# Kernel optimization log

Hardware: AMD Instinct MI355X
Metric: run time of the kernel (lower is better)

Reference implementation:

```python
import jax, jax.numpy as jnp
import numpy as np
import math

B, T, C, H, DFF = 4, 2048, 1024, 16, 4096
HD = C // H
EPS = 1e-5


def _layernorm(x, g, b):
    mu = jnp.mean(x, axis=-1, keepdims=True)
    var = jnp.var(x, axis=-1, keepdims=True)
    return (x - mu) * jax.lax.rsqrt(var + EPS) * g + b


def _new_gelu(x):
    # 0.5*x*(1+tanh(sqrt(2/pi)*(x+0.044715*x^3)))
    c = math.sqrt(2.0 / math.pi)
    return 0.5 * x * (1.0 + jnp.tanh(c * (x + 0.044715 * x ** 3)))


def setup_inputs() -> dict:
    key = jax.random.key(0)
    ks = jax.random.split(key, 12)
    s = lambda fan_in: 1.0 / math.sqrt(fan_in)
    return {
        "x": jax.random.normal(ks[0], (B, T, C), jnp.float32),
        "ln1_g": jnp.ones((C,), jnp.float32),
        "ln1_b": jnp.zeros((C,), jnp.float32),
        "w_qkv": jax.random.normal(ks[1], (C, 3 * C), jnp.float32) * s(C),
        "b_qkv": jnp.zeros((3 * C,), jnp.float32),
        "w_o": jax.random.normal(ks[2], (C, C), jnp.float32) * s(C),
        "b_o": jnp.zeros((C,), jnp.float32),
        "ln2_g": jnp.ones((C,), jnp.float32),
        "ln2_b": jnp.zeros((C,), jnp.float32),
        "w_fc": jax.random.normal(ks[3], (C, DFF), jnp.float32) * s(C),
        "b_fc": jnp.zeros((DFF,), jnp.float32),
        "w_proj": jax.random.normal(ks[4], (DFF, C), jnp.float32) * s(DFF),
        "b_proj": jnp.zeros((C,), jnp.float32),
    }


def reference(x, ln1_g, ln1_b, w_qkv, b_qkv, w_o, b_o, ln2_g, ln2_b, w_fc, b_fc, w_proj, b_proj):
    # --- attention sub-block ---
    h = _layernorm(x, ln1_g, ln1_b)
    qkv = h @ w_qkv + b_qkv                                  # (B,T,3C)
    q, k, v = jnp.split(qkv, 3, axis=-1)
    q = q.reshape(B, T, H, HD).transpose(0, 2, 1, 3)          # (B,H,T,hd)
    k = k.reshape(B, T, H, HD).transpose(0, 2, 1, 3)
    v = v.reshape(B, T, H, HD).transpose(0, 2, 1, 3)
    scores = jnp.einsum("bhqd,bhkd->bhqk", q, k) / math.sqrt(HD)
    causal = jnp.tril(jnp.ones((T, T), jnp.bool_))            # (T,T)
    scores = jnp.where(causal[None, None], scores, -jnp.inf)
    probs = jax.nn.softmax(scores, axis=-1)
    attn = jnp.einsum("bhqk,bhkd->bhqd", probs, v)
    attn = attn.transpose(0, 2, 1, 3).reshape(B, T, C)
    x = x + attn @ w_o + b_o
    # --- MLP sub-block ---
    h2 = _layernorm(x, ln2_g, ln2_b)
    x = x + _new_gelu(h2 @ w_fc + b_fc) @ w_proj + b_proj
    return x
```

## Files before the change

kernel.cpp:

```cpp
#include <hip/hip_runtime.h>
#include <hip/hip_bf16.h>

using bf16 = __hip_bfloat16;
typedef __attribute__((ext_vector_type(8))) short bf16x8;
typedef __attribute__((ext_vector_type(4))) float f32x4;
typedef __attribute__((ext_vector_type(16))) float f32x16;

#define LOG2E 1.4426950408889634f

__device__ inline short f2b(float f) {
  __hip_bfloat16 h = __float2bfloat16(f);
  return *reinterpret_cast<short*>(&h);
}
__device__ inline float b2f(short s) {
  unsigned int u = ((unsigned int)(unsigned short)s) << 16;
  float f;
  __builtin_memcpy(&f, &u, 4);
  return f;
}
__device__ inline unsigned pk2(float a, float b) {
  return (unsigned)(unsigned short)f2b(a) |
         ((unsigned)(unsigned short)f2b(b) << 16);
}

__global__ __launch_bounds__(256) void transpose_cast_kernel(
    const float* __restrict__ in, bf16* __restrict__ out, int K, int N) {
  __shared__ float tile[32][33];
  int tx = threadIdx.x & 31;
  int ty = threadIdx.x >> 5;
  int n0 = blockIdx.x * 32, k0 = blockIdx.y * 32;
#pragma unroll
  for (int i = 0; i < 4; i++)
    tile[ty + i * 8][tx] = in[(size_t)(k0 + ty + i * 8) * N + n0 + tx];
  __syncthreads();
#pragma unroll
  for (int i = 0; i < 4; i++)
    out[(size_t)(n0 + ty + i * 8) * K + k0 + tx] =
        __float2bfloat16(tile[tx][ty + i * 8]);
}

__global__ __launch_bounds__(256) void transpose_v_kernel(
    const bf16* __restrict__ qkv, bf16* __restrict__ vt) {
  __shared__ short tile[64][66];
  const int bh = blockIdx.y;
  const int b = bh >> 4, h = bh & 15;
  const int t0 = blockIdx.x * 64;
  const int tid = threadIdx.x;
  const int r = tid >> 3, c8 = (tid & 7) * 8;
#pragma unroll
  for (int p = 0; p < 2; p++) {
    int t = r + p * 32;
    bf16x8 v = *(const bf16x8*)&qkv[(size_t)(b * 2048 + t0 + t) * 3072 + 2048 +
                                    h * 64 + c8];
#pragma unroll
    for (int i = 0; i < 8; i++) tile[t][c8 + i] = v[i];
  }
  __syncthreads();
#pragma unroll
  for (int p = 0; p < 2; p++) {
    int d = r + p * 32;
    int tt = c8;
    bf16x8 o;
#pragma unroll
    for (int i = 0; i < 8; i++) o[i] = tile[tt + i][d];
    *(bf16x8*)&vt[(size_t)(bh * 64 + d) * 2048 + t0 + tt] = o;
  }
}

__global__ __launch_bounds__(256) void ln_kernel(
    const float* __restrict__ x, const float* __restrict__ g,
    const float* __restrict__ b, bf16* __restrict__ out) {
  int row = blockIdx.x;
  const float4 v = ((const float4*)(x + (size_t)row * 1024))[threadIdx.x];
  float s = v.x + v.y + v.z + v.w;
  float ss = v.x * v.x + v.y * v.y + v.z * v.z + v.w * v.w;
#pragma unroll
  for (int off = 1; off < 64; off <<= 1) {
    s += __shfl_xor(s, off);
    ss += __shfl_xor(ss, off);
  }
  __shared__ float red[2][4];
  int w = threadIdx.x >> 6, lane = threadIdx.x & 63;
  if (lane == 0) { red[0][w] = s; red[1][w] = ss; }
  __syncthreads();
  s = red[0][0] + red[0][1] + red[0][2] + red[0][3];
  ss = red[1][0] + red[1][1] + red[1][2] + red[1][3];
  float mu = s * (1.0f / 1024.0f);
  float var = ss * (1.0f / 1024.0f) - mu * mu;
  float rstd = rsqrtf(var + 1e-5f);
  const float4 gv = ((const float4*)g)[threadIdx.x];
  const float4 bv = ((const float4*)b)[threadIdx.x];
  short4 o4;
  o4.x = f2b((v.x - mu) * rstd * gv.x + bv.x);
  o4.y = f2b((v.y - mu) * rstd * gv.y + bv.y);
  o4.z = f2b((v.z - mu) * rstd * gv.z + bv.z);
  o4.w = f2b((v.w - mu) * rstd * gv.w + bv.w);
  ((short4*)out)[(size_t)row * 256 + threadIdx.x] = o4;
}

__global__ __launch_bounds__(256) void fused_ln_kernel(
    const float* __restrict__ p0, const float* __restrict__ p1,
    const float* __restrict__ bo, const float* __restrict__ x,
    const float* __restrict__ g, const float* __restrict__ bln,
    float* __restrict__ x1, bf16* __restrict__ h2) {
  int row = blockIdx.x;
  size_t base = (size_t)row * 256 + threadIdx.x;
  float4 a = ((const float4*)p0)[base];
  float4 c = ((const float4*)p1)[base];
  float4 xr = ((const float4*)x)[base];
  float4 bo4 = ((const float4*)bo)[threadIdx.x];
  float4 v;
  v.x = a.x + c.x + xr.x + bo4.x;
  v.y = a.y + c.y + xr.y + bo4.y;
  v.z = a.z + c.z + xr.z + bo4.z;
  v.w = a.w + c.w + xr.w + bo4.w;
  ((float4*)x1)[base] = v;
  float s = v.x + v.y + v.z + v.w;
  float ss = v.x * v.x + v.y * v.y + v.z * v.z + v.w * v.w;
#pragma unroll
  for (int off = 1; off < 64; off <<= 1) {
    s += __shfl_xor(s, off);
    ss += __shfl_xor(ss, off);
  }
  __shared__ float red[2][4];
  int w = threadIdx.x >> 6, lane = threadIdx.x & 63;
  if (lane == 0) { red[0][w] = s; red[1][w] = ss; }
  __syncthreads();
  s = red[0][0] + red[0][1] + red[0][2] + red[0][3];
  ss = red[1][0] + red[1][1] + red[1][2] + red[1][3];
  float mu = s * (1.0f / 1024.0f);
  float var = ss * (1.0f / 1024.0f) - mu * mu;
  float rstd = rsqrtf(var + 1e-5f);
  const float4 gv = ((const float4*)g)[threadIdx.x];
  const float4 bv = ((const float4*)bln)[threadIdx.x];
  short4 o4;
  o4.x = f2b((v.x - mu) * rstd * gv.x + bv.x);
  o4.y = f2b((v.y - mu) * rstd * gv.y + bv.y);
  o4.z = f2b((v.z - mu) * rstd * gv.z + bv.z);
  o4.w = f2b((v.w - mu) * rstd * gv.w + bv.w);
  ((short4*)h2)[base] = o4;
}

__global__ __launch_bounds__(256) void fused_add_kernel(
    float* __restrict__ out, const float* __restrict__ q1,
    const float* __restrict__ x1, const float* __restrict__ bp, int n4) {
  for (int i = blockIdx.x * 256 + threadIdx.x; i < n4; i += gridDim.x * 256) {
    float4 a = ((const float4*)out)[i];
    float4 c = ((const float4*)q1)[i];
    float4 xr = ((const float4*)x1)[i];
    float4 b4 = ((const float4*)bp)[i & 255];
    float4 v;
    v.x = a.x + c.x + xr.x + b4.x;
    v.y = a.y + c.y + xr.y + b4.y;
    v.z = a.z + c.z + xr.z + b4.z;
    v.w = a.w + c.w + xr.w + b4.w;
    ((float4*)out)[i] = v;
  }
}

template <int EPI>
__global__ __launch_bounds__(512, 1) void gemm256_kernel(
    const bf16* __restrict__ A, const bf16* __restrict__ Bt,
    const float* __restrict__ bias, float* __restrict__ out0,
    float* __restrict__ out1, void* __restrict__ outv, int M, int N, int Kfull,
    int Ksub, int ntiles) {
  __shared__ short As[2][256 * 64];
  __shared__ short Bs[2][256 * 64];
  const int tid = threadIdx.x;
  const int lane = tid & 63, wid = tid >> 6;
  const int wr = wid >> 2, wc = wid & 3;

  const int nwg = gridDim.x;
  const int flat = blockIdx.x;
  const int sw = (flat & 7) * (nwg >> 3) + (flat >> 3);
  const int kq = sw / ntiles;
  const int tile = sw % ntiles;
  const int gy = M >> 8;
  const int bcol = tile / gy, brow = tile % gy;
  const int koff = kq * Ksub;
  const int nk = Ksub >> 6;

  const int srow = tid >> 3;
  const int schs = (tid & 7) ^ (srow & 7);

  auto stA = [&](int kt, int buf) {
#pragma unroll
    for (int r = 0; r < 4; r++) {
      const bf16* src = A + (size_t)(brow * 256 + r * 64 + srow) * Kfull +
                        koff + kt * 64 + schs * 8;
      __builtin_amdgcn_global_load_lds(
          (const __attribute__((address_space(1))) unsigned int*)src,
          (__attribute__((address_space(3))) unsigned int*)
              &As[buf][(r * 64 + wid * 8) * 64],
          16, 0, 0);
    }
  };
  auto stB = [&](int kt, int buf) {
#pragma unroll
    for (int r = 0; r < 4; r++) {
      const bf16* src = Bt + (size_t)(bcol * 256 + r * 64 + srow) * Kfull +
                        koff + kt * 64 + schs * 8;
      __builtin_amdgcn_global_load_lds(
          (const __attribute__((address_space(1))) unsigned int*)src,
          (__attribute__((address_space(3))) unsigned int*)
              &Bs[buf][(r * 64 + wid * 8) * 64],
          16, 0, 0);
    }
  };

  f32x4 acc[8][4] = {};
  bf16x8 af[4][2], bfr[4][2];

  auto rdB = [&](int cur) {
#pragma unroll
    for (int nn = 0; nn < 4; nn++)
#pragma unroll
      for (int ks = 0; ks < 2; ks++) {
        const int row = wc * 64 + nn * 16 + (lane & 15);
        const int ch = (ks * 4 + (lane >> 4)) ^ (row & 7);
        bfr[nn][ks] = *(const bf16x8*)&Bs[cur][row * 64 + ch * 8];
      }
  };
  auto rdA = [&](int cur, int mh) {
#pragma unroll
    for (int mm = 0; mm < 4; mm++)
#pragma unroll
      for (int ks = 0; ks < 2; ks++) {
        const int row = wr * 128 + mh * 64 + mm * 16 + (lane & 15);
        const int ch = (ks * 4 + (lane >> 4)) ^ (row & 7);
        af[mm][ks] = *(const bf16x8*)&As[cur][row * 64 + ch * 8];
      }
  };

  stA(0, 0);
  stB(0, 0);
  asm volatile("s_waitcnt vmcnt(0)" ::: "memory");
  __builtin_amdgcn_s_barrier();

  for (int t = 0; t < nk; t++) {
    const int cur = t & 1, nxt = cur ^ 1;
    rdB(cur);
    rdA(cur, 0);
    if (t + 1 < nk) {
      stA(t + 1, nxt);
      stB(t + 1, nxt);
    }
    __builtin_amdgcn_s_barrier();
    asm volatile("s_waitcnt lgkmcnt(0)" ::: "memory");
    __builtin_amdgcn_sched_barrier(0);
    __builtin_amdgcn_s_setprio(1);
#pragma unroll
    for (int mm = 0; mm < 4; mm++)
#pragma unroll
      for (int nn = 0; nn < 4; nn++)
#pragma unroll
        for (int ks = 0; ks < 2; ks++)
          acc[mm][nn] = __builtin_amdgcn_mfma_f32_16x16x32_bf16(
              af[mm][ks], bfr[nn][ks], acc[mm][nn], 0, 0, 0);
    __builtin_amdgcn_s_setprio(0);
    __builtin_amdgcn_s_barrier();
    rdA(cur, 1);
    asm volatile("s_waitcnt lgkmcnt(0)" ::: "memory");
    __builtin_amdgcn_sched_barrier(0);
    __builtin_amdgcn_s_setprio(1);
#pragma unroll
    for (int mm = 0; mm < 4; mm++)
#pragma unroll
      for (int nn = 0; nn < 4; nn++)
#pragma unroll
        for (int ks = 0; ks < 2; ks++)
          acc[4 + mm][nn] = __builtin_amdgcn_mfma_f32_16x16x32_bf16(
              af[mm][ks], bfr[nn][ks], acc[4 + mm][nn], 0, 0, 0);
    __builtin_amdgcn_s_setprio(0);
    if (t + 1 < nk) asm volatile("s_waitcnt vmcnt(0)" ::: "memory");
    __builtin_amdgcn_s_barrier();
  }

#pragma unroll
  for (int m = 0; m < 8; m++)
#pragma unroll
    for (int n = 0; n < 4; n++) {
      int gr0 = brow * 256 + wr * 128 + m * 16 + (lane >> 4) * 4;
      int gc = bcol * 256 + wc * 64 + n * 16 + (lane & 15);
      if constexpr (EPI == 3) {
        float* po = kq ? out1 : out0;
#pragma unroll
        for (int j = 0; j < 4; j++)
          po[(size_t)(gr0 + j) * N + gc] = acc[m][n][j];
      } else {
        float bia = bias[gc];
#pragma unroll
        for (int j = 0; j < 4; j++) {
          float v = acc[m][n][j] + bia;
          size_t idx = (size_t)(gr0 + j) * N + gc;
          if constexpr (EPI == 0) {
            ((bf16*)outv)[idx] = __float2bfloat16(v);
          } else {
            float u = 0.7978845608028654f * (v + 0.044715f * v * v * v);
            float t2 = exp2f(u * (2.0f * LOG2E));
            float th = 1.0f - 2.0f / (t2 + 1.0f);
            ((bf16*)outv)[idx] = __float2bfloat16(0.5f * v * (1.0f + th));
          }
        }
      }
    }
}

__global__ __launch_bounds__(256) void attn_kernel(
    const bf16* __restrict__ qkv, const bf16* __restrict__ vt,
    bf16* __restrict__ attn) {
  const int bh = blockIdx.x;
  const int qt = blockIdx.y;
  const int b = bh >> 4, h = bh & 15;
  const int tid = threadIdx.x, w = tid >> 6, lane = tid & 63;
  const int col = lane & 31;
  const int hi = lane >> 5;

  __shared__ short Kl[64 * 64];
  __shared__ short Vl[64 * 64];

  const int qbase = qt * 128 + w * 32;
  const int qglob = qbase + col;
  const size_t qrow = (size_t)(b * 2048 + qglob);

  bf16x8 qf[4];
#pragma unroll
  for (int dks = 0; dks < 4; dks++) {
    bf16x8 raw =
        *(const bf16x8*)&qkv[qrow * 3072 + h * 64 + dks * 16 + hi * 8];
#pragma unroll
    for (int i = 0; i < 8; i++) qf[dks][i] = f2b(b2f(raw[i]) * 0.125f);
  }

  f32x16 ot[2] = {};
  float m = -1e30f, l = 0.0f;

  const int ktend = qt * 2 + 1;
  for (int kt = 0; kt <= ktend; kt++) {
    const int kv0 = kt * 64;
    __syncthreads();
#pragma unroll
    for (int j = 0; j < 2; j++) {
      int c = (j * 4 + w) * 64 + lane;
      int row = c >> 3;
      int sw8 = ((c & 7) ^ (row & 7)) * 8;
      const bf16* gk =
          qkv + (size_t)(b * 2048 + kv0 + row) * 3072 + 1024 + h * 64 + sw8;
      __builtin_amdgcn_global_load_lds(
          (const __attribute__((address_space(1))) unsigned int*)gk,
          (__attribute__((address_space(3))) unsigned int*)(Kl + (j * 4 + w) * 512),
          16, 0, 0);
      const bf16* gv = vt + (size_t)(bh * 64 + row) * 2048 + kv0 + sw8;
      __builtin_amdgcn_global_load_lds(
          (const __attribute__((address_space(1))) unsigned int*)gv,
          (__attribute__((address_space(3))) unsigned int*)(Vl + (j * 4 + w) * 512),
          16, 0, 0);
    }
    __syncthreads();

    if (kv0 <= qbase + 31) {
      f32x16 st[2] = {};
#pragma unroll
      for (int s = 0; s < 2; s++) {
        int kvrow = s * 32 + col;
        int swz = kvrow & 7;
#pragma unroll
        for (int dks = 0; dks < 4; dks++) {
          int ch = (dks * 2 + hi) ^ swz;
          bf16x8 kf = *(const bf16x8*)&Kl[kvrow * 64 + ch * 8];
          st[s] = __builtin_amdgcn_mfma_f32_32x32x16_bf16(kf, qf[dks], st[s],
                                                          0, 0, 0);
        }
      }
      if (kv0 + 63 > qbase) {
#pragma unroll
        for (int s = 0; s < 2; s++)
#pragma unroll
          for (int r = 0; r < 16; r++) {
            int kv = kv0 + s * 32 + (r & 3) + 8 * (r >> 2) + 4 * hi;
            if (kv > qglob) st[s][r] = -1e30f;
          }
      }
      float pmax = -1e30f;
#pragma unroll
      for (int s = 0; s < 2; s++)
#pragma unroll
        for (int r = 0; r < 16; r++) pmax = fmaxf(pmax, st[s][r]);
      pmax = fmaxf(pmax, __shfl_xor(pmax, 32));
      float mnew = fmaxf(m, pmax);
      float corr = exp2f((m - mnew) * LOG2E);
      m = mnew;
      float rs = 0.0f;
#pragma unroll
      for (int s = 0; s < 2; s++)
#pragma unroll
        for (int r = 0; r < 16; r++) {
          float pv = exp2f((st[s][r] - mnew) * LOG2E);
          st[s][r] = pv;
          rs += pv;
        }
      rs += __shfl_xor(rs, 32);
      l = l * corr + rs;
#pragma unroll
      for (int s = 0; s < 2; s++)
#pragma unroll
        for (int r = 0; r < 16; r++) ot[s][r] *= corr;

#pragma unroll
      for (int sub = 0; sub < 2; sub++) {
#pragma unroll
        for (int kl = 0; kl < 2; kl++) {
          unsigned A0 = pk2(st[sub][kl * 8 + 0], st[sub][kl * 8 + 1]);
          unsigned A1 = pk2(st[sub][kl * 8 + 2], st[sub][kl * 8 + 3]);
          unsigned B0 = pk2(st[sub][kl * 8 + 4], st[sub][kl * 8 + 5]);
          unsigned B1 = pk2(st[sub][kl * 8 + 6], st[sub][kl * 8 + 7]);
          unsigned sA0 = (unsigned)__shfl_xor((int)A0, 32);
          unsigned sA1 = (unsigned)__shfl_xor((int)A1, 32);
          unsigned sB0 = (unsigned)__shfl_xor((int)B0, 32);
          unsigned sB1 = (unsigned)__shfl_xor((int)B1, 32);
          union { unsigned u[4]; bf16x8 v; } pf;
          pf.u[0] = hi ? sB0 : A0;
          pf.u[1] = hi ? sB1 : A1;
          pf.u[2] = hi ? B0 : sA0;
          pf.u[3] = hi ? B1 : sA1;
          int ks = sub * 2 + kl;
#pragma unroll
          for (int ds = 0; ds < 2; ds++) {
            int drow = ds * 32 + col;
            int ch = (ks * 2 + hi) ^ (drow & 7);
            bf16x8 vf = *(const bf16x8*)&Vl[drow * 64 + ch * 8];
            ot[ds] = __builtin_amdgcn_mfma_f32_32x32x16_bf16(vf, pf.v, ot[ds],
                                                             0, 0, 0);
          }
        }
      }
    }
  }

  float rl = 1.0f / l;
#pragma unroll
  for (int ds = 0; ds < 2; ds++)
#pragma unroll
    for (int j = 0; j < 4; j++) {
      ushort4 o4;
      o4.x = (unsigned short)f2b(ot[ds][4 * j + 0] * rl);
      o4.y = (unsigned short)f2b(ot[ds][4 * j + 1] * rl);
      o4.z = (unsigned short)f2b(ot[ds][4 * j + 2] * rl);
      o4.w = (unsigned short)f2b(ot[ds][4 * j + 3] * rl);
      *(ushort4*)&attn[qrow * 1024 + h * 64 + 32 * ds + 8 * j + 4 * hi] = o4;
    }
}

extern "C" void kernel_launch(void* const* d_in, const int* in_sizes, int n_in,
                              void* d_out, int out_size, void* d_ws,
                              size_t ws_size, hipStream_t stream) {
  (void)in_sizes; (void)n_in; (void)out_size; (void)ws_size;
  const float* x      = (const float*)d_in[0];
  const float* ln1_g  = (const float*)d_in[1];
  const float* ln1_b  = (const float*)d_in[2];
  const float* w_qkv  = (const float*)d_in[3];
  const float* b_qkv  = (const float*)d_in[4];
  const float* w_o    = (const float*)d_in[5];
  const float* b_o    = (const float*)d_in[6];
  const float* ln2_g  = (const float*)d_in[7];
  const float* ln2_b  = (const float*)d_in[8];
  const float* w_fc   = (const float*)d_in[9];
  const float* b_fc   = (const float*)d_in[10];
  const float* w_proj = (const float*)d_in[11];
  const float* b_proj = (const float*)d_in[12];
  float* out = (float*)d_out;

  char* ws = (char*)d_ws;
  const size_t MB = 1048576;
  float* x1     = (float*)(ws + 0);
  bf16* slotA   = (bf16*)(ws + 32 * MB);
  bf16* wt_qkv  = (bf16*)(ws + 48 * MB);
  bf16* wt_o    = (bf16*)(ws + 54 * MB);
  bf16* wt_fc   = (bf16*)(ws + 56 * MB);
  bf16* wt_proj = (bf16*)(ws + 64 * MB);
  bf16* qkvb    = (bf16*)(ws + 72 * MB);
  bf16* vtb     = (bf16*)(ws + 120 * MB);
  float* p0     = (float*)(ws + 72 * MB);
  float* p1     = (float*)(ws + 104 * MB);
  bf16* gbuf    = (bf16*)(ws + 72 * MB);
  float* q1     = (float*)(ws + 32 * MB);

  dim3 blk(256);
  transpose_cast_kernel<<<dim3(3072 / 32, 1024 / 32), blk, 0, stream>>>(
      w_qkv, wt_qkv, 1024, 3072);
  transpose_cast_kernel<<<dim3(1024 / 32, 1024 / 32), blk, 0, stream>>>(
      w_o, wt_o, 1024, 1024);
  transpose_cast_kernel<<<dim3(4096 / 32, 1024 / 32), blk, 0, stream>>>(
      w_fc, wt_fc, 1024, 4096);
  transpose_cast_kernel<<<dim3(1024 / 32, 4096 / 32), blk, 0, stream>>>(
      w_proj, wt_proj, 4096, 1024);

  ln_kernel<<<8192, blk, 0, stream>>>(x, ln1_g, ln1_b, slotA);
  gemm256_kernel<0><<<dim3(384), dim3(512), 0, stream>>>(
      slotA, wt_qkv, b_qkv, nullptr, nullptr, qkvb, 8192, 3072, 1024, 1024,
      384);
  transpose_v_kernel<<<dim3(32, 64), blk, 0, stream>>>(qkvb, vtb);
  attn_kernel<<<dim3(64, 16), blk, 0, stream>>>(qkvb, vtb, slotA);
  gemm256_kernel<3><<<dim3(256), dim3(512), 0, stream>>>(
      slotA, wt_o, nullptr, p0, p1, nullptr, 8192, 1024, 1024, 512, 128);
  fused_ln_kernel<<<8192, blk, 0, stream>>>(p0, p1, b_o, x, ln2_g, ln2_b, x1,
                                            slotA);
  gemm256_kernel<2><<<dim3(512), dim3(512), 0, stream>>>(
      slotA, wt_fc, b_fc, nullptr, nullptr, gbuf, 8192, 4096, 1024, 1024, 512);
  gemm256_kernel<3><<<dim3(256), dim3(512), 0, stream>>>(
      gbuf, wt_proj, nullptr, out, q1, nullptr, 8192, 1024, 4096, 2048, 128);
  fused_add_kernel<<<dim3(2048), blk, 0, stream>>>(out, q1, x1, b_proj,
                                                   2097152);
}
```

Before: 444.7 us.

## Double-buffer attention K/V tiles, reverse q-tile order, and lazily rescale softmax

The attention kernel now prefetches the next K/V tile into a second LDS buffer while the current tile is computed. It waits on vmcnt instead of a full barrier before the loads, which hides global latency. Query tiles are launched in reverse order so the longest causal tiles start first, improving load balance. Softmax rescaling is skipped unless the running max grows by more than a threshold, and the max and sum reductions use trees. The cost is doubled LDS use, extra barriers, and some risk in the hand-written waitcnt and lazy-max numerics.

```diff
diff --git a/kernel.cpp b/kernel.cpp
--- a/kernel.cpp
+++ b/kernel.cpp
@@ -310,14 +310,14 @@
     const bf16* __restrict__ qkv, const bf16* __restrict__ vt,
     bf16* __restrict__ attn) {
   const int bh = blockIdx.x;
-  const int qt = blockIdx.y;
+  const int qt = 15 - blockIdx.y;
   const int b = bh >> 4, h = bh & 15;
   const int tid = threadIdx.x, w = tid >> 6, lane = tid & 63;
   const int col = lane & 31;
   const int hi = lane >> 5;
 
-  __shared__ short Kl[64 * 64];
-  __shared__ short Vl[64 * 64];
+  __shared__ short Kl[2][64 * 64];
+  __shared__ short Vl[2][64 * 64];
 
   const int qbase = qt * 128 + w * 32;
   const int qglob = qbase + col;
@@ -332,31 +332,44 @@
     for (int i = 0; i < 8; i++) qf[dks][i] = f2b(b2f(raw[i]) * 0.125f);
   }
 
-  f32x16 ot[2] = {};
-  float m = -1e30f, l = 0.0f;
-
-  const int ktend = qt * 2 + 1;
-  for (int kt = 0; kt <= ktend; kt++) {
-    const int kv0 = kt * 64;
-    __syncthreads();
+  auto stage = [&](int kt, int buf) {
+    const int kv0s = kt * 64;
 #pragma unroll
     for (int j = 0; j < 2; j++) {
       int c = (j * 4 + w) * 64 + lane;
       int row = c >> 3;
       int sw8 = ((c & 7) ^ (row & 7)) * 8;
       const bf16* gk =
-          qkv + (size_t)(b * 2048 + kv0 + row) * 3072 + 1024 + h * 64 + sw8;
+          qkv + (size_t)(b * 2048 + kv0s + row) * 3072 + 1024 + h * 64 + sw8;
       __builtin_amdgcn_global_load_lds(
           (const __attribute__((address_space(1))) unsigned int*)gk,
-          (__attribute__((address_space(3))) unsigned int*)(Kl + (j * 4 + w) * 512),
+          (__attribute__((address_space(3))) unsigned int*)(
+              &Kl[buf][(j * 4 + w) * 512]),
           16, 0, 0);
-      const bf16* gv = vt + (size_t)(bh * 64 + row) * 2048 + kv0 + sw8;
+      const bf16* gv = vt + (size_t)(bh * 64 + row) * 2048 + kv0s + sw8;
       __builtin_amdgcn_global_load_lds(
           (const __attribute__((address_space(1))) unsigned int*)gv,
-          (__attribute__((address_space(3))) unsigned int*)(Vl + (j * 4 + w) * 512),
+          (__attribute__((address_space(3))) unsigned int*)(
+              &Vl[buf][(j * 4 + w) * 512]),
           16, 0, 0);
     }
-    __syncthreads();
+  };
+
+  f32x16 ot[2] = {};
+  float m = -1e30f, l = 0.0f;
+
+  const int ktend = qt * 2 + 1;
+  stage(0, 0);
+  for (int kt = 0; kt <= ktend; kt++) {
+    const int kv0 = kt * 64;
+    const int cur = kt & 1;
+    if (kt < ktend) {
+      stage(kt + 1, cur ^ 1);
+      asm volatile("s_waitcnt vmcnt(4)" ::: "memory");
+    } else {
+      asm volatile("s_waitcnt vmcnt(0)" ::: "memory");
+    }
+    __builtin_amdgcn_s_barrier();
 
     if (kv0 <= qbase + 31) {
       f32x16 st[2] = {};
@@ -367,7 +380,7 @@
 #pragma unroll
         for (int dks = 0; dks < 4; dks++) {
           int ch = (dks * 2 + hi) ^ swz;
-          bf16x8 kf = *(const bf16x8*)&Kl[kvrow * 64 + ch * 8];
+          bf16x8 kf = *(const bf16x8*)&Kl[cur][kvrow * 64 + ch * 8];
           st[s] = __builtin_amdgcn_mfma_f32_32x32x16_bf16(kf, qf[dks], st[s],
                                                           0, 0, 0);
         }
@@ -381,30 +394,37 @@
             if (kv > qglob) st[s][r] = -1e30f;
           }
       }
-      float pmax = -1e30f;
+      float vm[16];
+#pragma unroll
+      for (int i = 0; i < 16; i++) vm[i] = fmaxf(st[0][i], st[1][i]);
+#pragma unroll
+      for (int w2 = 8; w2 >= 1; w2 >>= 1)
+#pragma unroll
+        for (int i = 0; i < w2; i++) vm[i] = fmaxf(vm[i], vm[i + w2]);
+      float pmax = fmaxf(vm[0], __shfl_xor(vm[0], 32));
+      if (!__all(pmax - m <= 8.0f)) {
+        float mnew = fmaxf(m, pmax);
+        float corr = exp2f((m - mnew) * LOG2E);
+        m = mnew;
+        l *= corr;
+#pragma unroll
+        for (int s = 0; s < 2; s++)
+#pragma unroll
+          for (int r = 0; r < 16; r++) ot[s][r] *= corr;
+      }
 #pragma unroll
       for (int s = 0; s < 2; s++)
 #pragma unroll
-        for (int r = 0; r < 16; r++) pmax = fmaxf(pmax, st[s][r]);
-      pmax = fmaxf(pmax, __shfl_xor(pmax, 32));
-      float mnew = fmaxf(m, pmax);
-      float corr = exp2f((m - mnew) * LOG2E);
-      m = mnew;
-      float rs = 0.0f;
-#pragma unroll
-      for (int s = 0; s < 2; s++)
-#pragma unroll
-        for (int r = 0; r < 16; r++) {
-          float pv = exp2f((st[s][r] - mnew) * LOG2E);
-          st[s][r] = pv;
-          rs += pv;
-        }
-      rs += __shfl_xor(rs, 32);
-      l = l * corr + rs;
-#pragma unroll
-      for (int s = 0; s < 2; s++)
-#pragma unroll
-        for (int r = 0; r < 16; r++) ot[s][r] *= corr;
+        for (int r = 0; r < 16; r++)
+          st[s][r] = exp2f((st[s][r] - m) * LOG2E);
+      float vs[16];
+#pragma unroll
+      for (int i = 0; i < 16; i++) vs[i] = st[0][i] + st[1][i];
+#pragma unroll
+      for (int w2 = 8; w2 >= 1; w2 >>= 1)
+#pragma unroll
+        for (int i = 0; i < w2; i++) vs[i] += vs[i + w2];
+      l += vs[0] + __shfl_xor(vs[0], 32);
 
 #pragma unroll
       for (int sub = 0; sub < 2; sub++) {
@@ -428,13 +448,14 @@
           for (int ds = 0; ds < 2; ds++) {
             int drow = ds * 32 + col;
             int ch = (ks * 2 + hi) ^ (drow & 7);
-            bf16x8 vf = *(const bf16x8*)&Vl[drow * 64 + ch * 8];
+            bf16x8 vf = *(const bf16x8*)&Vl[cur][drow * 64 + ch * 8];
             ot[ds] = __builtin_amdgcn_mfma_f32_32x32x16_bf16(vf, pf.v, ot[ds],
                                                              0, 0, 0);
           }
         }
       }
     }
+    __builtin_amdgcn_s_barrier();
   }
 
   float rl = 1.0f / l;
```

Measured after the change: 421.7 us. 1.05x faster.
